# Kernel optimization log

Measured on AMD Instinct MI355X. Metric: run time of the kernel, lower is better.

The kernel has to match this reference:

```python
import jax, jax.numpy as jnp
import numpy as np

N = 100000   # nodes
E = 1600000  # directed edges
B = 512      # graphs in batch
F = 9        # atom feature columns (OGB AtomEncoder)
V = 128      # vocab per atom feature
H = 256      # nhid
C = 10       # num_classes


def setup_inputs() -> dict:
    key = jax.random.key(0)
    ks = jax.random.split(key, 14)
    s = lambda k, shape: (jax.random.normal(k, shape, jnp.float32) * 0.05)
    return {
        "x": jax.random.randint(ks[0], (N, F), 0, V),
        "edge_index": jax.random.randint(ks[1], (2, E), 0, N),
        "batch": jnp.sort(jax.random.randint(ks[2], (N,), 0, B)),
        "atom_emb": s(ks[3], (F, V, H)),
        "W1": s(ks[4], (H, H)), "b1": s(ks[5], (H,)),
        "W2": s(ks[6], (H, H)), "b2": s(ks[7], (H,)),
        "W3": s(ks[8], (H, H)), "b3": s(ks[9], (H,)),
        "cw1": s(ks[10], (H, H // 2)), "cb1": s(ks[11], (H // 2,)),
        "cw2": s(ks[12], (H // 2, C)), "cb2": s(ks[13], (C,)),
    }


def reference(x, edge_index, batch, atom_emb, W1, b1, W2, b2, W3, b3, cw1, cb1, cw2, cb2):
    n = x.shape[0]
    # AtomEncoder: sum of per-column embeddings -> [N, H]
    h = atom_emb[jnp.arange(F)[None, :], x].sum(axis=1)

    # GCN normalization with self-loops (PyG GCNConv default)
    loop = jnp.arange(n, dtype=edge_index.dtype)
    row = jnp.concatenate([edge_index[0], loop])  # source
    col = jnp.concatenate([edge_index[1], loop])  # target
    deg = jax.ops.segment_sum(jnp.ones_like(col, jnp.float32), col, num_segments=n)
    dis = deg ** -0.5  # deg >= 1 because of self-loops
    norm = dis[row] * dis[col]  # [E+N]

    def gcn(feat, W, b):
        m = feat @ W                                   # [N, H]
        agg = jax.ops.segment_sum(norm[:, None] * m[row], col, num_segments=n)
        return agg + b

    x1 = jax.nn.relu(gcn(h, W1, b1))
    x2 = jax.nn.relu(gcn(x1, W2, b2))
    x3 = jax.nn.relu(gcn(x2, W3, b3))

    # global mean pool per graph, summed across the three layers
    counts = jax.ops.segment_sum(jnp.ones((n,), jnp.float32), batch, num_segments=B)
    pooled = jax.ops.segment_sum(x1 + x2 + x3, batch, num_segments=B) / counts[:, None]

    # classifier (dropout is identity in eval mode)
    hdn = jax.nn.relu(pooled @ cw1 + cb1)
    out = hdn @ cw2 + cb2
    return (out, 0)
```

## Files before the change

kernel.cpp:

```cpp
#include <hip/hip_runtime.h>
#include <hip/hip_bf16.h>
#include <cstdint>

#define HDIM 256
#define H2   128

using f32x4  = __attribute__((ext_vector_type(4))) float;
using bf16x8 = __attribute__((ext_vector_type(8))) short;
using u16x8  = __attribute__((ext_vector_type(8))) unsigned short;

__device__ inline unsigned short f2bf(float f) {
    unsigned x = __builtin_bit_cast(unsigned, f);
    return (unsigned short)((x + 0x7fffu + ((x >> 16) & 1u)) >> 16);
}
__device__ inline float bf2f(unsigned short u) {
    unsigned x = ((unsigned)u) << 16;
    return __builtin_bit_cast(float, x);
}

__global__ void k_deg(const int* __restrict__ col, int* __restrict__ deg0, int e) {
    int i = blockIdx.x * blockDim.x + threadIdx.x;
    if (i < e) atomicAdd(&deg0[col[i]], 1);
}

__global__ void k_scan1(const int* __restrict__ deg0, int* __restrict__ ptr,
                        int* __restrict__ bsum, int n) {
    __shared__ int sd[256];
    int i = blockIdx.x * 256 + threadIdx.x;
    int v = (i < n) ? deg0[i] : 0;
    sd[threadIdx.x] = v;
    __syncthreads();
    for (int off = 1; off < 256; off <<= 1) {
        int t = (threadIdx.x >= off) ? sd[threadIdx.x - off] : 0;
        __syncthreads();
        sd[threadIdx.x] += t;
        __syncthreads();
    }
    if (i < n) ptr[i] = sd[threadIdx.x] - v;
    if (threadIdx.x == 255) bsum[blockIdx.x] = sd[255];
}

__global__ void k_scan2(int* __restrict__ bsum, int nb) {
    __shared__ int sd[512];
    int t = threadIdx.x;
    int v = (t < nb) ? bsum[t] : 0;
    sd[t] = v;
    __syncthreads();
    for (int off = 1; off < 512; off <<= 1) {
        int x = (t >= off) ? sd[t - off] : 0;
        __syncthreads();
        sd[t] += x;
        __syncthreads();
    }
    if (t < nb) bsum[t] = sd[t] - v;
}

__global__ void k_scan3(int* __restrict__ ptr, const int* __restrict__ bsum,
                        const int* __restrict__ deg0, float* __restrict__ dis, int n) {
    int i = blockIdx.x * 256 + threadIdx.x;
    if (i < n) {
        ptr[i] += bsum[blockIdx.x];
        dis[i] = rsqrtf((float)deg0[i] + 1.0f);
    }
}

__global__ void k_fill(const int* __restrict__ row, const int* __restrict__ col,
                       const int* __restrict__ ptr, int* __restrict__ cursor,
                       int* __restrict__ csr_src, int e) {
    int i = blockIdx.x * blockDim.x + threadIdx.x;
    if (i < e) {
        int v = col[i];
        int s = atomicAdd(&cursor[v], 1);
        csr_src[ptr[v] + s] = row[i];
    }
}

__global__ void k_emb(const float* __restrict__ emb, short* __restrict__ embb, int tot) {
    int i = blockIdx.x * 256 + threadIdx.x;
    if (i < tot) embb[i] = (short)f2bf(emb[i]);
}

__global__ __launch_bounds__(256) void k_atom(const int* __restrict__ x,
                                              const short* __restrict__ embb,
                                              short* __restrict__ h,
                                              int n, int F, int V) {
    int node = blockIdx.x * 4 + (threadIdx.x >> 6);
    int lane = threadIdx.x & 63;
    if (node >= n) return;
    int xv = x[node * F + (lane < F ? lane : 0)];
    float acc[4] = {};
    for (int f = 0; f < F; ++f) {
        int idx = __shfl(xv, f, 64);
        ushort4 v = *(const ushort4*)((const unsigned short*)embb +
                                      ((size_t)(f * V + idx)) * HDIM + lane * 4);
        acc[0] += bf2f(v.x); acc[1] += bf2f(v.y);
        acc[2] += bf2f(v.z); acc[3] += bf2f(v.w);
    }
    ushort4 o = { f2bf(acc[0]), f2bf(acc[1]), f2bf(acc[2]), f2bf(acc[3]) };
    *(ushort4*)(h + (size_t)node * HDIM + lane * 4) = o;
}

__global__ void k_wt3(const float* __restrict__ W1, const float* __restrict__ W2,
                      const float* __restrict__ W3, short* __restrict__ Wt1,
                      short* __restrict__ Wt2, short* __restrict__ Wt3) {
    const float* W = (blockIdx.y == 0) ? W1 : (blockIdx.y == 1) ? W2 : W3;
    short* Wt      = (blockIdx.y == 0) ? Wt1 : (blockIdx.y == 1) ? Wt2 : Wt3;
    int i = blockIdx.x * 256 + threadIdx.x;
    int nn = i >> 8, k = i & 255;
    Wt[nn * HDIM + k] = (short)f2bf(W[k * HDIM + nn]);
}

__global__ __launch_bounds__(256, 4) void k_gemm(const short* __restrict__ A,
                                                 const short* __restrict__ Wt,
                                                 short* __restrict__ Co, int n) {
    __shared__ unsigned char As[64 * 512];
    int row0 = blockIdx.x * 64;
    int t = threadIdx.x;
    int wid  = t >> 6;
    int lane = t & 63;
#pragma unroll
    for (int j = 0; j < 8; ++j) {
        int c  = (wid * 8 + j) * 64 + lane;
        int r  = c >> 5;
        int cb = (c & 31) * 16;
        int gr = row0 + r; if (gr >= n) gr = n - 1;
        const unsigned int* g = (const unsigned int*)
            ((const char*)A + (size_t)gr * 512 + (cb ^ ((r & 7) << 4)));
        unsigned int* l = (unsigned int*)(As + (size_t)(wid * 8 + j) * 1024);
        __builtin_amdgcn_global_load_lds(g, l, 16, 0, 0);
    }
    __syncthreads();

    int lm = lane & 15;
    int kg = lane >> 4;
    int colw = wid * 64;
    f32x4 acc[4][4] = {};
#pragma unroll 2
    for (int kk = 0; kk < 8; ++kk) {
        bf16x8 a[4], b[4];
#pragma unroll
        for (int i = 0; i < 4; ++i) {
            int R = i * 16 + lm;
            int boff = (kk * 64 + kg * 16) ^ ((R & 7) << 4);
            a[i] = *(const bf16x8*)(As + R * 512 + boff);
        }
#pragma unroll
        for (int j = 0; j < 4; ++j) {
            int cidx = colw + j * 16 + lm;
            b[j] = *(const bf16x8*)(Wt + (size_t)cidx * HDIM + kk * 32 + kg * 8);
        }
#pragma unroll
        for (int i = 0; i < 4; ++i)
#pragma unroll
            for (int j = 0; j < 4; ++j)
                acc[i][j] = __builtin_amdgcn_mfma_f32_16x16x32_bf16(a[i], b[j], acc[i][j], 0, 0, 0);
    }
#pragma unroll
    for (int i = 0; i < 4; ++i)
#pragma unroll
        for (int j = 0; j < 4; ++j) {
            int c = colw + j * 16 + lm;
#pragma unroll
            for (int r4 = 0; r4 < 4; ++r4) {
                int r = row0 + i * 16 + kg * 4 + r4;
                if (r < n) Co[(size_t)r * HDIM + c] = (short)f2bf(acc[i][j][r4]);
            }
        }
}

__global__ __launch_bounds__(256) void k_agg(const short* __restrict__ mS,
                                             const int* __restrict__ csr_src,
                                             const int* __restrict__ ptr,
                                             const int* __restrict__ deg0,
                                             const float* __restrict__ dis,
                                             const float* __restrict__ bias,
                                             short* __restrict__ xout, int n) {
    int node = blockIdx.x * 4 + (threadIdx.x >> 6);
    if (node >= n) return;
    int lane = threadIdx.x & 63;
    int half = lane >> 5;
    int cl = lane & 31;
    const unsigned short* m = (const unsigned short*)mS;
    float dv = dis[node];
    float acc[8] = {};
    if (half == 0) {
        u16x8 r = *(const u16x8*)(m + (size_t)node * HDIM + cl * 8);
        float sw = dv * dv;
#pragma unroll
        for (int j = 0; j < 8; ++j) acc[j] = sw * bf2f(r[j]);
    }
    int start = ptr[node];
    int cnt = deg0[node];
    for (int base = 0; base < cnt; base += 64) {
        int mm = cnt - base; if (mm > 64) mm = 64;
        int uu = 0; float du = 0.f;
        if (lane < mm) {
            uu = __builtin_nontemporal_load(&csr_src[start + base + lane]);
            du = dis[uu];
        }
        int nst = (mm + 7) >> 3;
        for (int s = 0; s < nst; ++s) {
            u16x8 r[4]; float w[4];
#pragma unroll
            for (int q = 0; q < 4; ++q) {
                int i = 8 * s + 2 * q + half;
                int u   = __shfl(uu, i & 63, 64);
                float ww = dv * __shfl(du, i & 63, 64);
                bool v = i < mm;
                w[q] = v ? ww : 0.f;
                r[q] = *(const u16x8*)(m + (size_t)(v ? u : 0) * HDIM + cl * 8);
            }
#pragma unroll
            for (int q = 0; q < 4; ++q)
#pragma unroll
                for (int j = 0; j < 8; ++j) acc[j] += w[q] * bf2f(r[q][j]);
        }
    }
#pragma unroll
    for (int j = 0; j < 8; ++j) acc[j] += __shfl_xor(acc[j], 32, 64);
    if (half == 0) {
        const float4 b0 = *(const float4*)(bias + cl * 8);
        const float4 b1 = *(const float4*)(bias + cl * 8 + 4);
        float bb[8] = {b0.x, b0.y, b0.z, b0.w, b1.x, b1.y, b1.z, b1.w};
        u16x8 o;
#pragma unroll
        for (int j = 0; j < 8; ++j)
            o[j] = f2bf(fmaxf(acc[j] + bb[j], 0.f));
        *(u16x8*)((unsigned short*)xout + (size_t)node * HDIM + cl * 8) = o;
    }
}

__global__ __launch_bounds__(256) void k_pool(const short* __restrict__ x1,
                                              const short* __restrict__ x2,
                                              const short* __restrict__ x3,
                                              const int* __restrict__ batch,
                                              float* __restrict__ partial,
                                              int n, int B) {
    __shared__ float spool[8][HDIM];
    int g = blockIdx.x, seg = blockIdx.y, t = threadIdx.x;
    int cg = t & 31, rl = t >> 5;
    auto lb = [&](int key) {
        int lo = 0, hi = n;
        while (lo < hi) { int mid = (lo + hi) >> 1; if (batch[mid] < key) lo = mid + 1; else hi = mid; }
        return lo;
    };
    int lo = lb(g), hi = lb(g + 1);
    int len = hi - lo;
    int per = (len + 3) >> 2;
    int s0 = lo + seg * per;
    int s1 = s0 + per; if (s1 > hi) s1 = hi;
    float acc[8] = {};
    for (int r = s0 + rl; r < s1; r += 8) {
        size_t base = (size_t)r * HDIM + cg * 8;
        u16x8 a = *(const u16x8*)((const unsigned short*)x1 + base);
        u16x8 b = *(const u16x8*)((const unsigned short*)x2 + base);
        u16x8 c = *(const u16x8*)((const unsigned short*)x3 + base);
#pragma unroll
        for (int j = 0; j < 8; ++j)
            acc[j] += bf2f(a[j]) + bf2f(b[j]) + bf2f(c[j]);
    }
#pragma unroll
    for (int j = 0; j < 8; ++j) spool[rl][cg * 8 + j] = acc[j];
    __syncthreads();
    float s = 0.f;
#pragma unroll
    for (int r2 = 0; r2 < 8; ++r2) s += spool[r2][t];
    partial[(size_t)(seg * B + g) * HDIM + t] = s;
}

__global__ __launch_bounds__(256) void k_cls(const float* __restrict__ partial,
                                             const int* __restrict__ batch,
                                             const float* __restrict__ cw1,
                                             const float* __restrict__ cb1,
                                             const float* __restrict__ cw2,
                                             const float* __restrict__ cb2,
                                             float* __restrict__ out,
                                             int n, int B, int C) {
    __shared__ float sp[HDIM];
    __shared__ float sh[H2];
    int g = blockIdx.x, t = threadIdx.x;
    auto lb = [&](int key) {
        int lo = 0, hi = n;
        while (lo < hi) { int mid = (lo + hi) >> 1; if (batch[mid] < key) lo = mid + 1; else hi = mid; }
        return lo;
    };
    int lo = lb(g), hi = lb(g + 1);
    int cnt = hi - lo; if (cnt < 1) cnt = 1;
    float s = 0.f;
#pragma unroll
    for (int seg = 0; seg < 4; ++seg)
        s += partial[(size_t)(seg * B + g) * HDIM + t];
    sp[t] = s / (float)cnt;
    __syncthreads();
    if (t < H2) {
        float a = cb1[t];
        for (int h = 0; h < HDIM; ++h) a += sp[h] * cw1[h * H2 + t];
        sh[t] = fmaxf(a, 0.f);
    }
    __syncthreads();
    if (t < C) {
        float o = cb2[t];
        for (int j = 0; j < H2; ++j) o += sh[j] * cw2[j * C + t];
        out[g * C + t] = o;
    }
    if (g == 0 && t == 0) out[B * C] = 0.f;
}

extern "C" void kernel_launch(void* const* d_in, const int* in_sizes, int n_in,
                              void* d_out, int out_size, void* d_ws, size_t ws_size,
                              hipStream_t stream) {
    const int* x      = (const int*)d_in[0];
    const int* erow   = (const int*)d_in[1];
    const int* batch  = (const int*)d_in[2];
    const float* emb  = (const float*)d_in[3];
    const float* W1   = (const float*)d_in[4];
    const float* b1   = (const float*)d_in[5];
    const float* W2   = (const float*)d_in[6];
    const float* b2   = (const float*)d_in[7];
    const float* W3   = (const float*)d_in[8];
    const float* b3   = (const float*)d_in[9];
    const float* cw1  = (const float*)d_in[10];
    const float* cb1  = (const float*)d_in[11];
    const float* cw2  = (const float*)d_in[12];
    const float* cb2  = (const float*)d_in[13];
    float* out = (float*)d_out;

    const int N = in_sizes[2];
    const int E = in_sizes[1] / 2;
    const int F = in_sizes[0] / N;
    const int V = in_sizes[3] / (F * HDIM);
    const int C = in_sizes[13];
    const int B = (out_size - 1) / C;
    const int* ecol = erow + E;
    const int EMBTOT = F * V * HDIM;

    char* w = (char*)d_ws;
    auto carve = [&](size_t bytes) {
        void* p = (void*)w;
        w += (bytes + 255) & ~(size_t)255;
        return p;
    };
    short* P0     = (short*)carve((size_t)N * HDIM * 2);
    short* P1     = (short*)carve((size_t)N * HDIM * 2);
    short* P2     = (short*)carve((size_t)N * HDIM * 2);
    short* mS     = (short*)carve((size_t)N * HDIM * 2);
    short* embb   = (short*)carve((size_t)EMBTOT * 2);
    short* Wt1    = (short*)carve((size_t)HDIM * HDIM * 2);
    short* Wt2    = (short*)carve((size_t)HDIM * HDIM * 2);
    short* Wt3    = (short*)carve((size_t)HDIM * HDIM * 2);
    float* partial= (float*)carve((size_t)4 * B * HDIM * 4);
    float* dis    = (float*)carve((size_t)N * 4);
    int* deg0     = (int*)carve((size_t)N * 4);
    int* ptr      = (int*)carve((size_t)N * 4);
    int* cursor   = (int*)carve((size_t)N * 4);
    int* bsum     = (int*)carve(1024 * 4);
    int* csr      = (int*)carve((size_t)E * 4);

    int nblk = (N + 255) / 256;

    hipMemsetAsync(deg0, 0, (size_t)N * 4, stream);
    hipMemsetAsync(cursor, 0, (size_t)N * 4, stream);
    k_deg<<<(E + 255) / 256, 256, 0, stream>>>(ecol, deg0, E);
    k_scan1<<<nblk, 256, 0, stream>>>(deg0, ptr, bsum, N);
    k_scan2<<<1, 512, 0, stream>>>(bsum, nblk);
    k_scan3<<<nblk, 256, 0, stream>>>(ptr, bsum, deg0, dis, N);
    k_fill<<<(E + 255) / 256, 256, 0, stream>>>(erow, ecol, ptr, cursor, csr, E);
    k_emb<<<(EMBTOT + 255) / 256, 256, 0, stream>>>(emb, embb, EMBTOT);
    dim3 wgrid(HDIM, 3);
    k_wt3<<<wgrid, 256, 0, stream>>>(W1, W2, W3, Wt1, Wt2, Wt3);
    k_atom<<<(N + 3) / 4, 256, 0, stream>>>(x, embb, P0, N, F, V);

    int ggrid = (N + 63) / 64;
    int agrid = (N + 3) / 4;

    k_gemm<<<ggrid, 256, 0, stream>>>(P0, Wt1, mS, N);
    k_agg<<<agrid, 256, 0, stream>>>(mS, csr, ptr, deg0, dis, b1, P1, N);
    k_gemm<<<ggrid, 256, 0, stream>>>(P1, Wt2, mS, N);
    k_agg<<<agrid, 256, 0, stream>>>(mS, csr, ptr, deg0, dis, b2, P2, N);
    k_gemm<<<ggrid, 256, 0, stream>>>(P2, Wt3, mS, N);
    k_agg<<<agrid, 256, 0, stream>>>(mS, csr, ptr, deg0, dis, b3, P0, N);

    dim3 pgrid(B, 4);
    k_pool<<<pgrid, 256, 0, stream>>>(P1, P2, P0, batch, partial, N, B);
    k_cls<<<B, 256, 0, stream>>>(partial, batch, cw1, cb1, cw2, cb2, out, N, B, C);
}
```

Baseline: 768.0 us.

## Build CSR via coarse bucketing plus per-bucket LDS counting sort

Replaces the per-edge scattered atomic fill of the CSR with two passes. The first pass counts degrees and appends packed (src,dst) pairs into fixed-capacity buckets of 256 destination nodes. The second pass places each bucket's edges in shared memory and writes its CSR segment contiguously. This aims to cut random global atomics and scattered writes, at the cost of an extra 8-byte-per-edge buffer round trip and heavily contended per-bucket atomics. Edges beyond the fixed bucket capacity would be silently dropped.

After: 1.215 ms. 58.2% more time.

```diff
diff --git a/kernel.cpp b/kernel.cpp
--- a/kernel.cpp
+++ b/kernel.cpp
@@ -4,6 +4,8 @@
 
 #define HDIM 256
 #define H2   128
+#define BCAP 4608
+#define SCAP 4608
 
 using f32x4  = __attribute__((ext_vector_type(4))) float;
 using bf16x8 = __attribute__((ext_vector_type(8))) short;
@@ -18,9 +20,17 @@
     return __builtin_bit_cast(float, x);
 }
 
-__global__ void k_deg(const int* __restrict__ col, int* __restrict__ deg0, int e) {
+__global__ void k_bucket(const int* __restrict__ row, const int* __restrict__ col,
+                         int* __restrict__ deg0, int* __restrict__ bcur,
+                         unsigned long long* __restrict__ buckets, int e) {
     int i = blockIdx.x * blockDim.x + threadIdx.x;
-    if (i < e) atomicAdd(&deg0[col[i]], 1);
+    if (i >= e) return;
+    int c = col[i], r = row[i];
+    atomicAdd(&deg0[c], 1);
+    int b = c >> 8;
+    int s = atomicAdd(&bcur[b], 1);
+    if (s < BCAP)
+        buckets[(size_t)b * BCAP + s] = ((unsigned long long)(unsigned)r << 32) | (unsigned)c;
 }
 
 __global__ void k_scan1(const int* __restrict__ deg0, int* __restrict__ ptr,
@@ -64,15 +74,32 @@
     }
 }
 
-__global__ void k_fill(const int* __restrict__ row, const int* __restrict__ col,
-                       const int* __restrict__ ptr, int* __restrict__ cursor,
-                       int* __restrict__ csr_src, int e) {
-    int i = blockIdx.x * blockDim.x + threadIdx.x;
-    if (i < e) {
-        int v = col[i];
-        int s = atomicAdd(&cursor[v], 1);
-        csr_src[ptr[v] + s] = row[i];
-    }
+__global__ __launch_bounds__(256) void k_sort(const unsigned long long* __restrict__ buckets,
+                                              const int* __restrict__ bcur,
+                                              const int* __restrict__ ptr,
+                                              int* __restrict__ csr,
+                                              int n, int etot) {
+    __shared__ int stage[SCAP];
+    __shared__ int lcur[256];
+    int b = blockIdx.x, t = threadIdx.x;
+    int v0 = b << 8;
+    int v1 = v0 + 256; if (v1 > n) v1 = n;
+    lcur[t] = 0;
+    __syncthreads();
+    int base = ptr[v0];
+    int end  = (v1 < n) ? ptr[v1] : etot;
+    int span = end - base; if (span > SCAP) span = SCAP;
+    int bc = bcur[b]; if (bc > BCAP) bc = BCAP;
+    for (int i = t; i < bc; i += 256) {
+        unsigned long long en = buckets[(size_t)b * BCAP + i];
+        int c = (int)(en & 0xffffffffu);
+        int r = (int)(en >> 32);
+        int off = atomicAdd(&lcur[c & 255], 1);
+        int pos = ptr[c] - base + off;
+        if (pos < SCAP) stage[pos] = r;
+    }
+    __syncthreads();
+    for (int j = t; j < span; j += 256) csr[base + j] = stage[j];
 }
 
 __global__ void k_emb(const float* __restrict__ emb, short* __restrict__ embb, int tot) {
@@ -333,6 +360,7 @@
     const int B = (out_size - 1) / C;
     const int* ecol = erow + E;
     const int EMBTOT = F * V * HDIM;
+    const int NB = (N + 255) >> 8;
 
     char* w = (char*)d_ws;
     auto carve = [&](size_t bytes) {
@@ -352,19 +380,21 @@
     float* dis    = (float*)carve((size_t)N * 4);
     int* deg0     = (int*)carve((size_t)N * 4);
     int* ptr      = (int*)carve((size_t)N * 4);
-    int* cursor   = (int*)carve((size_t)N * 4);
+    int* bcur     = (int*)carve((size_t)NB * 4);
     int* bsum     = (int*)carve(1024 * 4);
     int* csr      = (int*)carve((size_t)E * 4);
+    unsigned long long* buckets =
+        (unsigned long long*)carve((size_t)NB * BCAP * 8);
 
     int nblk = (N + 255) / 256;
 
     hipMemsetAsync(deg0, 0, (size_t)N * 4, stream);
-    hipMemsetAsync(cursor, 0, (size_t)N * 4, stream);
-    k_deg<<<(E + 255) / 256, 256, 0, stream>>>(ecol, deg0, E);
+    hipMemsetAsync(bcur, 0, (size_t)NB * 4, stream);
+    k_bucket<<<(E + 255) / 256, 256, 0, stream>>>(erow, ecol, deg0, bcur, buckets, E);
     k_scan1<<<nblk, 256, 0, stream>>>(deg0, ptr, bsum, N);
     k_scan2<<<1, 512, 0, stream>>>(bsum, nblk);
     k_scan3<<<nblk, 256, 0, stream>>>(ptr, bsum, deg0, dis, N);
-    k_fill<<<(E + 255) / 256, 256, 0, stream>>>(erow, ecol, ptr, cursor, csr, E);
+    k_sort<<<NB, 256, 0, stream>>>(buckets, bcur, ptr, csr, N, E);
     k_emb<<<(EMBTOT + 255) / 256, 256, 0, stream>>>(emb, embb, EMBTOT);
     dim3 wgrid(HDIM, 3);
     k_wt3<<<wgrid, 256, 0, stream>>>(W1, W2, W3, Wt1, Wt2, Wt3);
```
